# Kernel tuning notes

Hardware: AMD Instinct MI355X
Metric: run time of the kernel (lower is better)

## Reference

```python
import jax, jax.numpy as jnp
import numpy as np

TEMPERATURE = 0.07
BASE_TEMPERATURE = 0.07


def setup_inputs() -> dict:
    key = jax.random.key(0)
    k1, k2 = jax.random.split(key)
    features = jax.random.normal(k1, (4096, 2, 128), dtype=jnp.float32)
    labels = jax.random.randint(k2, (4096,), 0, 100, dtype=jnp.int64)
    return {"features": features, "labels": labels}


def reference(features, labels):
    # features: [B, n_views, D], labels: [B]
    B, n_views, D = features.shape
    N = B * n_views

    # label equality mask [B, B]
    lab = labels.reshape(-1, 1)
    mask = (lab == lab.T).astype(jnp.float32)

    # flatten views (C-order, same as torch .view) and L2-normalize
    feat = features.reshape(N, D)
    feat = feat / jnp.clip(jnp.linalg.norm(feat, axis=1, keepdims=True), 1e-12)

    # similarity logits [N, N]
    logits = jnp.matmul(feat, feat.T) / TEMPERATURE
    logits_max = jax.lax.stop_gradient(jnp.max(logits, axis=1, keepdims=True))
    logits = logits - logits_max

    # tile mask to [N, N] (torch .repeat ordering) and remove self-contrast
    mask = jnp.tile(mask, (n_views, n_views))
    logits_mask = 1.0 - jnp.eye(N, dtype=jnp.float32)
    mask = mask * logits_mask

    exp_logits = jnp.exp(logits) * logits_mask
    log_prob = logits - jnp.log(jnp.sum(exp_logits, axis=1, keepdims=True) + 1e-12)

    mask_pos_pairs = jnp.clip(jnp.sum(mask, axis=1), 1.0)
    mean_log_prob_pos = jnp.sum(mask * log_prob, axis=1) / mask_pos_pairs

    loss = -(TEMPERATURE / BASE_TEMPERATURE) * mean_log_prob_pos
    return jnp.mean(loss.reshape(n_views, B))
```

## Files before the change

kernel.cpp:

```cpp
#include <hip/hip_runtime.h>
#include <hip/hip_bf16.h>
#include <hip/hip_fp8.h>
#include <math.h>

#define NB 4096
#define NN 8192
#define DD 128
#define NCLS 100
#define NSPLIT 16

constexpr float INV_T = 14.285714285714286f;
constexpr float EC1   = 20.609929155556620f;
constexpr float EC0   = -20.609929155556620f;
constexpr float LN2   = 0.6931471805599453f;

typedef unsigned char u8;
typedef __attribute__((ext_vector_type(8))) int   v8i;
typedef __attribute__((ext_vector_type(4))) int   v4i;
typedef __attribute__((ext_vector_type(4))) float f32x4;


__global__ __launch_bounds__(256) void k_norm(const float* __restrict__ feat,
                                              u8* __restrict__ fb8,
                                              float* __restrict__ selfdot,
                                              float* __restrict__ out) {
    const int gid = blockIdx.x * 256 + threadIdx.x;
    if (gid == 0) out[0] = 0.0f;
    const int r    = gid >> 6;
    const int lane = threadIdx.x & 63;
    const float2 v = ((const float2*)(feat + (size_t)r * DD))[lane];
    float ss = v.x * v.x + v.y * v.y;
#pragma unroll
    for (int off = 1; off < 64; off <<= 1) ss += __shfl_xor(ss, off, 64);
    const float scale = 1.0f / fmaxf(sqrtf(ss), 1e-12f);
    const __hip_fp8_e4m3 qx(v.x * scale), qy(v.y * scale);
    const unsigned short pack = (unsigned short)qx.__x |
                                ((unsigned short)qy.__x << 8);
    const int g    = r >> 4;
    const int n15r = r & 15;
    const int qc   = lane >> 4;
    const int hc   = (lane >> 3) & 1;
    const int bofs = (2 * lane) & 15;
    *(unsigned short*)(fb8 + (size_t)g * 2048 + hc * 1024 +
                       ((qc * 16 + n15r) << 4) + bofs) = pack;
    const float xb = (float)qx, yb = (float)qy;
    float s2 = xb * xb + yb * yb;
#pragma unroll
    for (int off = 1; off < 64; off <<= 1) s2 += __shfl_xor(s2, off, 64);
    if (lane == 0) selfdot[r] = s2;
}

__global__ __launch_bounds__(256, 4) void k_main(const u8* __restrict__ fb8,
                                                 const int* __restrict__ labels,
                                                 float* __restrict__ g_se,
                                                 float* __restrict__ g_ps) {
    __shared__ int slab[512];

    const int tid  = threadIdx.x;
    const int lane = tid & 63;
    const int w    = tid >> 6;
    const int rb   = blockIdx.x >> 4;
    const int js   = blockIdx.x & (NSPLIT - 1);
    const int i0   = rb * 128 + w * 32;
    const int jb0  = js * 512;
    const int q    = lane >> 4;
    const int n15  = lane & 15;

    slab[tid]       = labels[(jb0 + tid) & (NB - 1)];
    slab[tid + 256] = labels[(jb0 + tid + 256) & (NB - 1)];

    v8i af[2];
#pragma unroll
    for (int tt = 0; tt < 2; ++tt) {
        const u8* ap = fb8 + (size_t)((i0 >> 4) + tt) * 2048 + lane * 16;
        const v4i lo = *(const v4i*)ap;
        const v4i hi = *(const v4i*)(ap + 1024);
        v8i a;
#pragma unroll
        for (int k = 0; k < 4; ++k) { a[k] = lo[k]; a[4 + k] = hi[k]; }
        af[tt] = a;
    }
    int labi[8];
#pragma unroll
    for (int tt = 0; tt < 2; ++tt)
#pragma unroll
        for (int r = 0; r < 4; ++r)
            labi[tt * 4 + r] = labels[(i0 + tt * 16 + q * 4 + r) & (NB - 1)];

    float a_se[8] = {}, a_ps[8] = {};

    __syncthreads();

    const u8* bbase = fb8 + (size_t)(jb0 >> 4) * 2048 + lane * 16;
#pragma unroll 4
    for (int jt = 0; jt < 32; ++jt) {
        const u8* bp = bbase + (size_t)jt * 2048;
        const v4i lo = *(const v4i*)bp;
        const v4i hi = *(const v4i*)(bp + 1024);
        v8i bb;
#pragma unroll
        for (int k = 0; k < 4; ++k) { bb[k] = lo[k]; bb[4 + k] = hi[k]; }
        const int labj = slab[jt * 16 + n15];
        f32x4 a0 = {0.f, 0.f, 0.f, 0.f}, a1 = {0.f, 0.f, 0.f, 0.f};
        a0 = __builtin_amdgcn_mfma_scale_f32_16x16x128_f8f6f4(
                 af[0], bb, a0, 0, 0, 0, 0x7F7F7F7F, 0, 0x7F7F7F7F);
        a1 = __builtin_amdgcn_mfma_scale_f32_16x16x128_f8f6f4(
                 af[1], bb, a1, 0, 0, 0, 0x7F7F7F7F, 0, 0x7F7F7F7F);
#pragma unroll
        for (int r = 0; r < 4; ++r) {
            const float d0 = a0[r], d1 = a1[r];
            a_se[r]     += __builtin_amdgcn_exp2f(fmaf(d0, EC1, EC0));
            a_se[4 + r] += __builtin_amdgcn_exp2f(fmaf(d1, EC1, EC0));
            a_ps[r]     += (labi[r]     == labj) ? d0 : 0.0f;
            a_ps[4 + r] += (labi[4 + r] == labj) ? d1 : 0.0f;
        }
    }

#pragma unroll
    for (int s = 0; s < 8; ++s) {
        float v1 = a_se[s], v2 = a_ps[s];
#pragma unroll
        for (int off = 1; off < 16; off <<= 1) {
            v1 += __shfl_xor(v1, off, 64);
            v2 += __shfl_xor(v2, off, 64);
        }
        if (n15 == 0) {
            const int row = i0 + (s >> 2) * 16 + q * 4 + (s & 3);
            g_se[js * NN + row] = v1;
            g_ps[js * NN + row] = v2;
        }
    }
}

__global__ __launch_bounds__(256) void k_final(const int* __restrict__ labels,
                                               const float* __restrict__ g_se,
                                               const float* __restrict__ g_ps,
                                               const float* __restrict__ selfdot,
                                               float* __restrict__ out) {
    __shared__ int hist[NCLS];
    const int tid = threadIdx.x;
    for (int i = tid; i < NCLS; i += 256) hist[i] = 0;
    __syncthreads();
    for (int b = tid; b < NB; b += 256) atomicAdd(&hist[labels[b]], 1);
    __syncthreads();

    const int r = blockIdx.x * 256 + tid;
    const int c = labels[r & (NB - 1)];
    float se = 0.f, ps = 0.f;
#pragma unroll
    for (int t = 0; t < NSPLIT; ++t) {
        se += g_se[t * NN + r];
        ps += g_ps[t * NN + r];
    }
    const float sd = selfdot[r];
    se -= __builtin_amdgcn_exp2f(fmaf(sd, EC1, EC0));
    const float ct = (float)(2 * hist[c] - 1);
    const float possum = INV_T * ((ps - sd) - ct);
    const float lg  = __builtin_amdgcn_logf(se + 1e-12f) * LN2;
    const float mlpp = (possum - ct * lg) / fmaxf(ct, 1.0f);
    float v = -mlpp * (1.0f / (float)NN);
#pragma unroll
    for (int off = 1; off < 64; off <<= 1) v += __shfl_xor(v, off, 64);
    __shared__ float sred[4];
    if ((tid & 63) == 0) sred[tid >> 6] = v;
    __syncthreads();
    if (tid == 0) atomicAdd(out, sred[0] + sred[1] + sred[2] + sred[3]);
}

extern "C" void kernel_launch(void* const* d_in, const int* in_sizes, int n_in,
                              void* d_out, int out_size, void* d_ws, size_t ws_size,
                              hipStream_t stream) {
    const float* feat = (const float*)d_in[0];
    const int* labels = (const int*)d_in[1];
    float* out        = (float*)d_out;
    char* ws          = (char*)d_ws;

    u8* fb8         = (u8*)ws;
    float* g_se     = (float*)(ws + (size_t)1 * 1024 * 1024);
    float* g_ps     = g_se + NSPLIT * NN;
    float* selfdot  = g_ps + NSPLIT * NN;

    k_norm<<<NN / 4, 256, 0, stream>>>(feat, fb8, selfdot, out);
    k_main<<<(NN / 128) * NSPLIT, 256, 0, stream>>>(fb8, labels, g_se, g_ps);
    k_final<<<NN / 256, 256, 0, stream>>>(labels, g_se, g_ps, selfdot, out);
}
```

Measured before the change: 80.84 us.

## Compute positive-pair logit sums via per-class feature sums instead of masked accumulation

The masked positive-logit accumulation in the main GEMM loop is replaced by per-class feature sums built with atomics in the normalize kernel. The final kernel then dots each row with its class sum. This removes label loads, compares and the second reduction from the hot loop, and halves the partial-sum traffic. In exchange it adds a memset and 8192x128 float atomics into 100x128 bins, which may contend, plus a 128-element dot product per row in the final kernel.

```diff
diff --git a/kernel.cpp b/kernel.cpp
--- a/kernel.cpp
+++ b/kernel.cpp
@@ -21,8 +21,10 @@
 
 
 __global__ __launch_bounds__(256) void k_norm(const float* __restrict__ feat,
+                                              const int* __restrict__ labels,
                                               u8* __restrict__ fb8,
                                               float* __restrict__ selfdot,
+                                              float* __restrict__ S,
                                               float* __restrict__ out) {
     const int gid = blockIdx.x * 256 + threadIdx.x;
     if (gid == 0) out[0] = 0.0f;
@@ -48,14 +50,13 @@
 #pragma unroll
     for (int off = 1; off < 64; off <<= 1) s2 += __shfl_xor(s2, off, 64);
     if (lane == 0) selfdot[r] = s2;
+    const int c = labels[r & (NB - 1)];
+    atomicAdd(&S[c * DD + 2 * lane],     xb);
+    atomicAdd(&S[c * DD + 2 * lane + 1], yb);
 }
 
 __global__ __launch_bounds__(256, 4) void k_main(const u8* __restrict__ fb8,
-                                                 const int* __restrict__ labels,
-                                                 float* __restrict__ g_se,
-                                                 float* __restrict__ g_ps) {
-    __shared__ int slab[512];
-
+                                                 float* __restrict__ g_se) {
     const int tid  = threadIdx.x;
     const int lane = tid & 63;
     const int w    = tid >> 6;
@@ -65,9 +66,6 @@
     const int jb0  = js * 512;
     const int q    = lane >> 4;
     const int n15  = lane & 15;
-
-    slab[tid]       = labels[(jb0 + tid) & (NB - 1)];
-    slab[tid + 256] = labels[(jb0 + tid + 256) & (NB - 1)];
 
     v8i af[2];
 #pragma unroll
@@ -80,16 +78,8 @@
         for (int k = 0; k < 4; ++k) { a[k] = lo[k]; a[4 + k] = hi[k]; }
         af[tt] = a;
     }
-    int labi[8];
-#pragma unroll
-    for (int tt = 0; tt < 2; ++tt)
-#pragma unroll
-        for (int r = 0; r < 4; ++r)
-            labi[tt * 4 + r] = labels[(i0 + tt * 16 + q * 4 + r) & (NB - 1)];
 
-    float a_se[8] = {}, a_ps[8] = {};
-
-    __syncthreads();
+    float a_se[8] = {};
 
     const u8* bbase = fb8 + (size_t)(jb0 >> 4) * 2048 + lane * 16;
 #pragma unroll 4
@@ -100,7 +90,6 @@
         v8i bb;
 #pragma unroll
         for (int k = 0; k < 4; ++k) { bb[k] = lo[k]; bb[4 + k] = hi[k]; }
-        const int labj = slab[jt * 16 + n15];
         f32x4 a0 = {0.f, 0.f, 0.f, 0.f}, a1 = {0.f, 0.f, 0.f, 0.f};
         a0 = __builtin_amdgcn_mfma_scale_f32_16x16x128_f8f6f4(
                  af[0], bb, a0, 0, 0, 0, 0x7F7F7F7F, 0, 0x7F7F7F7F);
@@ -108,33 +97,27 @@
                  af[1], bb, a1, 0, 0, 0, 0x7F7F7F7F, 0, 0x7F7F7F7F);
 #pragma unroll
         for (int r = 0; r < 4; ++r) {
-            const float d0 = a0[r], d1 = a1[r];
-            a_se[r]     += __builtin_amdgcn_exp2f(fmaf(d0, EC1, EC0));
-            a_se[4 + r] += __builtin_amdgcn_exp2f(fmaf(d1, EC1, EC0));
-            a_ps[r]     += (labi[r]     == labj) ? d0 : 0.0f;
-            a_ps[4 + r] += (labi[4 + r] == labj) ? d1 : 0.0f;
+            a_se[r]     += __builtin_amdgcn_exp2f(fmaf(a0[r], EC1, EC0));
+            a_se[4 + r] += __builtin_amdgcn_exp2f(fmaf(a1[r], EC1, EC0));
         }
     }
 
 #pragma unroll
     for (int s = 0; s < 8; ++s) {
-        float v1 = a_se[s], v2 = a_ps[s];
+        float v1 = a_se[s];
 #pragma unroll
-        for (int off = 1; off < 16; off <<= 1) {
-            v1 += __shfl_xor(v1, off, 64);
-            v2 += __shfl_xor(v2, off, 64);
-        }
+        for (int off = 1; off < 16; off <<= 1) v1 += __shfl_xor(v1, off, 64);
         if (n15 == 0) {
             const int row = i0 + (s >> 2) * 16 + q * 4 + (s & 3);
             g_se[js * NN + row] = v1;
-            g_ps[js * NN + row] = v2;
         }
     }
 }
 
 __global__ __launch_bounds__(256) void k_final(const int* __restrict__ labels,
                                                const float* __restrict__ g_se,
-                                               const float* __restrict__ g_ps,
+                                               const u8* __restrict__ fb8,
+                                               const float* __restrict__ S,
                                                const float* __restrict__ selfdot,
                                                float* __restrict__ out) {
     __shared__ int hist[NCLS];
@@ -146,12 +129,27 @@
 
     const int r = blockIdx.x * 256 + tid;
     const int c = labels[r & (NB - 1)];
-    float se = 0.f, ps = 0.f;
+    float se = 0.f;
 #pragma unroll
-    for (int t = 0; t < NSPLIT; ++t) {
-        se += g_se[t * NN + r];
-        ps += g_ps[t * NN + r];
-    }
+    for (int t = 0; t < NSPLIT; ++t) se += g_se[t * NN + r];
+
+    const int g    = r >> 4;
+    const int n15r = r & 15;
+    const float* Sc = S + c * DD;
+    float ps = 0.f;
+#pragma unroll
+    for (int qc = 0; qc < 4; ++qc)
+#pragma unroll
+        for (int h = 0; h < 2; ++h) {
+            const u8* bp = fb8 + (size_t)g * 2048 + h * 1024 + ((qc * 16 + n15r) << 4);
+            const int kb = qc * 32 + h * 16;
+#pragma unroll
+            for (int b = 0; b < 16; ++b) {
+                __hip_fp8_e4m3 f; f.__x = bp[b];
+                ps = fmaf((float)f, Sc[kb + b], ps);
+            }
+        }
+
     const float sd = selfdot[r];
     se -= __builtin_amdgcn_exp2f(fmaf(sd, EC1, EC0));
     const float ct = (float)(2 * hist[c] - 1);
@@ -177,10 +175,11 @@
 
     u8* fb8         = (u8*)ws;
     float* g_se     = (float*)(ws + (size_t)1 * 1024 * 1024);
-    float* g_ps     = g_se + NSPLIT * NN;
-    float* selfdot  = g_ps + NSPLIT * NN;
+    float* selfdot  = g_se + NSPLIT * NN;
+    float* S        = selfdot + NN;
 
-    k_norm<<<NN / 4, 256, 0, stream>>>(feat, fb8, selfdot, out);
-    k_main<<<(NN / 128) * NSPLIT, 256, 0, stream>>>(fb8, labels, g_se, g_ps);
-    k_final<<<NN / 256, 256, 0, stream>>>(labels, g_se, g_ps, selfdot, out);
+    hipMemsetAsync(S, 0, NCLS * DD * sizeof(float), stream);
+    k_norm<<<NN / 4, 256, 0, stream>>>(feat, labels, fb8, selfdot, S, out);
+    k_main<<<(NN / 128) * NSPLIT, 256, 0, stream>>>(fb8, g_se);
+    k_final<<<NN / 256, 256, 0, stream>>>(labels, g_se, fb8, S, selfdot, out);
 }
```

New measurement: 89.22 us. 10.4% more time.

## Fuse final reduction into main kernel via atomics and last-block pattern

Applied to the files above, without the earlier changes.

Drops the separate finalize kernel. Per-split partial sums are now accumulated with global float atomics into per-row accumulators, and the last block to finish (found through an atomic counter) computes the loss and writes the output. This removes one kernel launch and the scattered partial-sum buffers. In exchange it adds atomic contention, makes the float summation order nondeterministic, and leaves a serial tail where one block processes all 8192 rows.

```diff
diff --git a/kernel.cpp b/kernel.cpp
--- a/kernel.cpp
+++ b/kernel.cpp
@@ -8,6 +8,7 @@
 #define DD 128
 #define NCLS 100
 #define NSPLIT 16
+#define NBLK 1024
 
 constexpr float INV_T = 14.285714285714286f;
 constexpr float EC1   = 20.609929155556620f;
@@ -23,9 +24,13 @@
 __global__ __launch_bounds__(256) void k_norm(const float* __restrict__ feat,
                                               u8* __restrict__ fb8,
                                               float* __restrict__ selfdot,
+                                              float* __restrict__ se_acc,
+                                              float* __restrict__ ps_acc,
+                                              unsigned int* __restrict__ counter,
                                               float* __restrict__ out) {
     const int gid = blockIdx.x * 256 + threadIdx.x;
-    if (gid == 0) out[0] = 0.0f;
+    if (gid == 0) { out[0] = 0.0f; *counter = 0u; }
+    if (gid < NN) { se_acc[gid] = 0.0f; ps_acc[gid] = 0.0f; }
     const int r    = gid >> 6;
     const int lane = threadIdx.x & 63;
     const float2 v = ((const float2*)(feat + (size_t)r * DD))[lane];
@@ -52,9 +57,13 @@
 
 __global__ __launch_bounds__(256, 4) void k_main(const u8* __restrict__ fb8,
                                                  const int* __restrict__ labels,
-                                                 float* __restrict__ g_se,
-                                                 float* __restrict__ g_ps) {
+                                                 float* __restrict__ se_acc,
+                                                 float* __restrict__ ps_acc,
+                                                 const float* __restrict__ selfdot,
+                                                 unsigned int* __restrict__ counter,
+                                                 float* __restrict__ out) {
     __shared__ int slab[512];
+    __shared__ int amLast;
 
     const int tid  = threadIdx.x;
     const int lane = tid & 63;
@@ -126,45 +135,47 @@
         }
         if (n15 == 0) {
             const int row = i0 + (s >> 2) * 16 + q * 4 + (s & 3);
-            g_se[js * NN + row] = v1;
-            g_ps[js * NN + row] = v2;
+            atomicAdd(&se_acc[row], v1);
+            atomicAdd(&ps_acc[row], v2);
         }
     }
-}
 
-__global__ __launch_bounds__(256) void k_final(const int* __restrict__ labels,
-                                               const float* __restrict__ g_se,
-                                               const float* __restrict__ g_ps,
-                                               const float* __restrict__ selfdot,
-                                               float* __restrict__ out) {
-    __shared__ int hist[NCLS];
-    const int tid = threadIdx.x;
+    __threadfence();
+    __syncthreads();
+    if (tid == 0) amLast = (atomicAdd(counter, 1u) == NBLK - 1u);
+    __syncthreads();
+    if (!amLast) return;
+    __threadfence();
+
+    int* hist = slab;
+    float* sred = (float*)&slab[128];
     for (int i = tid; i < NCLS; i += 256) hist[i] = 0;
     __syncthreads();
     for (int b = tid; b < NB; b += 256) atomicAdd(&hist[labels[b]], 1);
     __syncthreads();
 
-    const int r = blockIdx.x * 256 + tid;
-    const int c = labels[r & (NB - 1)];
-    float se = 0.f, ps = 0.f;
+    float acc = 0.0f;
+#pragma unroll 4
+    for (int it = 0; it < NN / 256; ++it) {
+        const int r = it * 256 + tid;
+        const int c = labels[r & (NB - 1)];
+        float se = __hip_atomic_load(&se_acc[r], __ATOMIC_RELAXED,
+                                     __HIP_MEMORY_SCOPE_AGENT);
+        float ps = __hip_atomic_load(&ps_acc[r], __ATOMIC_RELAXED,
+                                     __HIP_MEMORY_SCOPE_AGENT);
+        const float sd = selfdot[r];
+        se -= __builtin_amdgcn_exp2f(fmaf(sd, EC1, EC0));
+        const float ct = (float)(2 * hist[c] - 1);
+        const float possum = INV_T * ((ps - sd) - ct);
+        const float lg  = __builtin_amdgcn_logf(se + 1e-12f) * LN2;
+        const float mlpp = (possum - ct * lg) / fmaxf(ct, 1.0f);
+        acc += -mlpp * (1.0f / (float)NN);
+    }
 #pragma unroll
-    for (int t = 0; t < NSPLIT; ++t) {
-        se += g_se[t * NN + r];
-        ps += g_ps[t * NN + r];
-    }
-    const float sd = selfdot[r];
-    se -= __builtin_amdgcn_exp2f(fmaf(sd, EC1, EC0));
-    const float ct = (float)(2 * hist[c] - 1);
-    const float possum = INV_T * ((ps - sd) - ct);
-    const float lg  = __builtin_amdgcn_logf(se + 1e-12f) * LN2;
-    const float mlpp = (possum - ct * lg) / fmaxf(ct, 1.0f);
-    float v = -mlpp * (1.0f / (float)NN);
-#pragma unroll
-    for (int off = 1; off < 64; off <<= 1) v += __shfl_xor(v, off, 64);
-    __shared__ float sred[4];
-    if ((tid & 63) == 0) sred[tid >> 6] = v;
+    for (int off = 1; off < 64; off <<= 1) acc += __shfl_xor(acc, off, 64);
+    if ((tid & 63) == 0) sred[tid >> 6] = acc;
     __syncthreads();
-    if (tid == 0) atomicAdd(out, sred[0] + sred[1] + sred[2] + sred[3]);
+    if (tid == 0) out[0] = sred[0] + sred[1] + sred[2] + sred[3];
 }
 
 extern "C" void kernel_launch(void* const* d_in, const int* in_sizes, int n_in,
@@ -175,12 +186,14 @@
     float* out        = (float*)d_out;
     char* ws          = (char*)d_ws;
 
-    u8* fb8         = (u8*)ws;
-    float* g_se     = (float*)(ws + (size_t)1 * 1024 * 1024);
-    float* g_ps     = g_se + NSPLIT * NN;
-    float* selfdot  = g_ps + NSPLIT * NN;
+    u8* fb8              = (u8*)ws;
+    float* se_acc        = (float*)(ws + (size_t)1 * 1024 * 1024);
+    float* ps_acc        = se_acc + NN;
+    float* selfdot       = ps_acc + NN;
+    unsigned int* counter = (unsigned int*)(selfdot + NN);
 
-    k_norm<<<NN / 4, 256, 0, stream>>>(feat, fb8, selfdot, out);
-    k_main<<<(NN / 128) * NSPLIT, 256, 0, stream>>>(fb8, labels, g_se, g_ps);
-    k_final<<<NN / 256, 256, 0, stream>>>(labels, g_se, g_ps, selfdot, out);
+    k_norm<<<NN / 4, 256, 0, stream>>>(feat, fb8, selfdot, se_acc, ps_acc,
+                                       counter, out);
+    k_main<<<NBLK, 256, 0, stream>>>(fb8, labels, se_acc, ps_acc, selfdot,
+                                     counter, out);
 }
```

Result: slower. 143.8 us (+77.9%).
